# Kernel tuning notes

Hardware: AMD Instinct MI355X
Metric: run time of the kernel (lower is better)

## Reference

```python
import jax, jax.numpy as jnp
import numpy as np

N = 50000       # nodes
E = 800000      # edges (before self-loops)
IN_DIM = 8
H = 4           # heads (layers 1-2)
D = 32          # per-head hidden dim
HD = H * D      # 128
BN_EPS = 1e-5
NEG_SLOPE = 0.2


def _gat_conv(x, src, dst, W, a_src, a_dst, b, heads, concat):
    """PyG-style GATConv (eval mode, self-loops already in src/dst)."""
    n = x.shape[0]
    h = (x @ W).reshape(n, heads, -1)                      # [N, H, D]
    al_s = jnp.einsum('nhd,hd->nh', h, a_src)              # [N, H]
    al_d = jnp.einsum('nhd,hd->nh', h, a_dst)              # [N, H]
    e = jax.nn.leaky_relu(al_s[src] + al_d[dst], NEG_SLOPE)  # [E', H]
    m = jax.ops.segment_max(e, dst, num_segments=n)
    m = jnp.where(jnp.isfinite(m), m, 0.0)
    ex = jnp.exp(e - m[dst])
    den = jax.ops.segment_sum(ex, dst, num_segments=n)
    alpha = ex / (den[dst] + 1e-16)                        # [E', H] neighborhood softmax
    out = jax.ops.segment_sum(alpha[:, :, None] * h[src], dst, num_segments=n)  # [N, H, D]
    out = out.reshape(n, -1) if concat else out.mean(axis=1)
    return out + b


def _bn(x, g, b, m, v):
    return (x - m) * jax.lax.rsqrt(v + BN_EPS) * g + b


def setup_inputs() -> dict:
    key = jax.random.key(0)
    ks = jax.random.split(key, 32)
    f32 = jnp.float32
    d = {}
    d['x'] = jax.random.normal(ks[0], (N, IN_DIM), dtype=f32)
    d['edge_index'] = jax.random.randint(ks[1], (2, E), 0, N, dtype=jnp.int64)
    # layer 1: GAT(8 -> 32, 4 heads, concat)
    d['W1'] = jax.random.normal(ks[2], (IN_DIM, HD), dtype=f32) * 0.3
    d['as1'] = jax.random.normal(ks[3], (H, D), dtype=f32) * 0.3
    d['ad1'] = jax.random.normal(ks[4], (H, D), dtype=f32) * 0.3
    d['b1'] = jax.random.normal(ks[5], (HD,), dtype=f32) * 0.1
    d['g1'] = 1.0 + 0.1 * jax.random.normal(ks[6], (HD,), dtype=f32)
    d['be1'] = 0.1 * jax.random.normal(ks[7], (HD,), dtype=f32)
    d['m1'] = 0.1 * jax.random.normal(ks[8], (HD,), dtype=f32)
    d['v1'] = jax.random.uniform(ks[9], (HD,), dtype=f32, minval=0.5, maxval=1.5)
    # layer 2: GAT(128 -> 32, 4 heads, concat)
    d['W2'] = jax.random.normal(ks[10], (HD, HD), dtype=f32) * 0.1
    d['as2'] = jax.random.normal(ks[11], (H, D), dtype=f32) * 0.3
    d['ad2'] = jax.random.normal(ks[12], (H, D), dtype=f32) * 0.3
    d['b2'] = jax.random.normal(ks[13], (HD,), dtype=f32) * 0.1
    d['g2'] = 1.0 + 0.1 * jax.random.normal(ks[14], (HD,), dtype=f32)
    d['be2'] = 0.1 * jax.random.normal(ks[15], (HD,), dtype=f32)
    d['m2'] = 0.1 * jax.random.normal(ks[16], (HD,), dtype=f32)
    d['v2'] = jax.random.uniform(ks[17], (HD,), dtype=f32, minval=0.5, maxval=1.5)
    # layer 3: GAT(128 -> 32, 1 head, no concat)
    d['W3'] = jax.random.normal(ks[18], (HD, D), dtype=f32) * 0.1
    d['as3'] = jax.random.normal(ks[19], (1, D), dtype=f32) * 0.3
    d['ad3'] = jax.random.normal(ks[20], (1, D), dtype=f32) * 0.3
    d['b3'] = jax.random.normal(ks[21], (D,), dtype=f32) * 0.1
    d['g3'] = 1.0 + 0.1 * jax.random.normal(ks[22], (D,), dtype=f32)
    d['be3'] = 0.1 * jax.random.normal(ks[23], (D,), dtype=f32)
    d['m3'] = 0.1 * jax.random.normal(ks[24], (D,), dtype=f32)
    d['v3'] = jax.random.uniform(ks[25], (D,), dtype=f32, minval=0.5, maxval=1.5)
    # classifier: Linear(32->16) -> ReLU -> Linear(16->1)
    d['cW1'] = jax.random.normal(ks[26], (D, 16), dtype=f32) * 0.2
    d['cb1'] = 0.1 * jax.random.normal(ks[27], (16,), dtype=f32)
    d['cW2'] = jax.random.normal(ks[28], (16, 1), dtype=f32) * 0.2
    d['cb2'] = 0.1 * jax.random.normal(ks[29], (1,), dtype=f32)
    return d


def reference(x, edge_index, W1, as1, ad1, b1, g1, be1, m1, v1,
              W2, as2, ad2, b2, g2, be2, m2, v2,
              W3, as3, ad3, b3, g3, be3, m3, v3,
              cW1, cb1, cW2, cb2):
    n = x.shape[0]
    loop = jnp.arange(n, dtype=edge_index.dtype)
    src = jnp.concatenate([edge_index[0], loop])   # PyG adds self-loops
    dst = jnp.concatenate([edge_index[1], loop])
    x1 = jax.nn.elu(_bn(_gat_conv(x, src, dst, W1, as1, ad1, b1, H, True), g1, be1, m1, v1))
    x2 = jax.nn.elu(_bn(_gat_conv(x1, src, dst, W2, as2, ad2, b2, H, True), g2, be2, m2, v2))
    x3 = jax.nn.elu(_bn(_gat_conv(x2, src, dst, W3, as3, ad3, b3, 1, False), g3, be3, m3, v3))
    hidden = jax.nn.relu(x3 @ cW1 + cb1)
    return jax.nn.sigmoid(hidden @ cW2 + cb2)      # [N, 1]
```

## Files before the change

kernel.cpp:

```cpp
#include <hip/hip_runtime.h>
#include <hip/hip_bf16.h>

#define BN_EPS 1e-5f
#define CAPB 6144
#define LOG2E 1.4426950408889634f

typedef unsigned short ushort_t;
typedef __attribute__((ext_vector_type(2))) float f32x2;

__device__ __forceinline__ float blo(unsigned w) { unsigned t = w << 16; return __builtin_bit_cast(float, t); }
__device__ __forceinline__ float bhi(unsigned w) { unsigned t = w & 0xffff0000u; return __builtin_bit_cast(float, t); }
__device__ __forceinline__ unsigned packbf2(float a, float b) {
  unsigned lo = (unsigned)__builtin_bit_cast(unsigned short, __float2bfloat16(a));
  unsigned hi = (unsigned)__builtin_bit_cast(unsigned short, __float2bfloat16(b));
  return lo | (hi << 16);
}
__device__ __forceinline__ float fexp2(float x) {
#if __has_builtin(__builtin_amdgcn_exp2f)
  return __builtin_amdgcn_exp2f(x);
#else
  return exp2f(x);
#endif
}
__device__ __forceinline__ void pkfma(f32x2& d, f32x2 a, f32x2 b) {
  asm("v_pk_fma_f32 %0, %1, %2, %0" : "+v"(d) : "v"(a), "v"(b));
}


__global__ __launch_bounds__(256) void k_binit(int* __restrict__ gCur, int nb) {
  int i = blockIdx.x * 256 + threadIdx.x;
  if (i < nb) gCur[i] = i * CAPB;
}

__global__ __launch_bounds__(256) void k_bucket(const int* __restrict__ ei, int E, int etot,
                                                unsigned* __restrict__ bkt, int* __restrict__ gCur,
                                                int nb) {
  __shared__ int sm[256];
  __shared__ int lstart[256];
  __shared__ int lcur[256];
  __shared__ int gbase[256];
  __shared__ unsigned stage[1024];
  int tid = threadIdx.x;
  int base = blockIdx.x * 1024;
  int cnt = etot - base; if (cnt > 1024) cnt = 1024;

  sm[tid] = 0;
  __syncthreads();
  unsigned key[4]; int have[4];
  #pragma unroll
  for (int u = 0; u < 4; ++u) {
    int idx = tid + u * 256;
    have[u] = (idx < cnt);
    if (have[u]) {
      int i = base + idx;
      int s, d;
      if (i < E) { s = ei[i]; d = ei[E + i]; }
      else       { s = i - E; d = s; }
      unsigned k = ((unsigned)d << 16) | (unsigned)s;
      key[u] = k;
      atomicAdd(&sm[k >> 24], 1);
    }
  }
  __syncthreads();
  int myc = sm[tid];
  #pragma unroll
  for (int off = 1; off < 256; off <<= 1) {
    int t = sm[tid];
    int u = (tid >= off) ? sm[tid - off] : 0;
    __syncthreads();
    sm[tid] = t + u;
    __syncthreads();
  }
  int excl = sm[tid] - myc;
  lstart[tid] = excl;
  lcur[tid] = excl;
  if (tid < nb) gbase[tid] = atomicAdd(&gCur[tid], myc);
  __syncthreads();
  #pragma unroll
  for (int u = 0; u < 4; ++u) {
    if (have[u]) {
      int bin = key[u] >> 24;
      int pos = atomicAdd(&lcur[bin], 1);
      stage[pos] = key[u];
    }
  }
  __syncthreads();
  for (int j = tid; j < cnt; j += 256) {
    unsigned k = stage[j];
    int bin = k >> 24;
    bkt[(size_t)gbase[bin] + (j - lstart[bin])] = k;
  }
}

__global__ __launch_bounds__(256) void k_csr(const unsigned* __restrict__ bkt,
                                             const int* __restrict__ gCur,
                                             int* __restrict__ csr, int* __restrict__ offs,
                                             int n, int nb, int etot) {
  __shared__ int sm[256];
  __shared__ int lstart[256];
  __shared__ int lcur[256];
  __shared__ unsigned itm[CAPB];
  __shared__ ushort_t limg[CAPB];
  int tid = threadIdx.x, b = blockIdx.x;
  int cnt = gCur[b] - b * CAPB;

  int c = 0;
  if (tid < nb) c = gCur[tid] - tid * CAPB;
  sm[tid] = c;
  __syncthreads();
  #pragma unroll
  for (int off = 1; off < 256; off <<= 1) {
    int t = sm[tid];
    int u = (tid >= off) ? sm[tid - off] : 0;
    __syncthreads();
    sm[tid] = t + u;
    __syncthreads();
  }
  int gbase = sm[b] - cnt;
  __syncthreads();

  sm[tid] = 0;
  __syncthreads();
  for (int j = tid; j < cnt; j += 256) {
    unsigned k = bkt[(size_t)b * CAPB + j];
    itm[j] = k;
    atomicAdd(&sm[(k >> 16) & 255], 1);
  }
  __syncthreads();
  int myc = sm[tid];
  #pragma unroll
  for (int off = 1; off < 256; off <<= 1) {
    int t = sm[tid];
    int u = (tid >= off) ? sm[tid - off] : 0;
    __syncthreads();
    sm[tid] = t + u;
    __syncthreads();
  }
  int excl = sm[tid] - myc;
  lstart[tid] = excl;
  lcur[tid] = excl;
  __syncthreads();
  for (int j = tid; j < cnt; j += 256) {
    unsigned k = itm[j];
    int d = (k >> 16) & 255;
    int pos = atomicAdd(&lcur[d], 1);
    limg[pos] = (ushort_t)(k & 0xffffu);
  }
  __syncthreads();
  for (int j = tid; j < cnt; j += 256) csr[gbase + j] = (int)limg[j];
  int gd = b * 256 + tid;
  if (gd < n) offs[gd] = gbase + lstart[tid];
  if (b == nb - 1 && tid == 0) offs[n] = etot;
}


template<int K, int FOUT, int HEADS, int BK>
__global__ __launch_bounds__(256) void k_gemm_t(const float* __restrict__ X,
    const float* __restrict__ W, const float* __restrict__ a_s, const float* __restrict__ a_d,
    ushort_t* __restrict__ Hout, float* __restrict__ als, float* __restrict__ ald, int n) {
  constexpr int BM = 128;
  constexpr int CT = FOUT / 8;
  constexpr int RT = 256 / CT;
  constexpr int TM = BM / RT;
  __shared__ float Xl[BK][BM];
  __shared__ float Wl[BK][FOUT];

  int tid = threadIdx.x;
  int ct = tid % CT, rt = tid / CT;
  int row0 = blockIdx.x * BM;

  float acc[TM][8];
  #pragma unroll
  for (int i = 0; i < TM; ++i)
    #pragma unroll
    for (int j = 0; j < 8; ++j) acc[i][j] = 0.f;

  for (int k0 = 0; k0 < K; k0 += BK) {
    constexpr int TPR = BK / 4;
    for (int s = tid; s < BM * TPR; s += 256) {
      int r = s / TPR, c4 = (s % TPR) * 4;
      float4 v = make_float4(0.f, 0.f, 0.f, 0.f);
      int grow = row0 + r;
      if (grow < n) v = *(const float4*)&X[(size_t)grow * K + k0 + c4];
      Xl[c4 + 0][r] = v.x; Xl[c4 + 1][r] = v.y; Xl[c4 + 2][r] = v.z; Xl[c4 + 3][r] = v.w;
    }
    for (int s = tid; s < BK * (FOUT / 4); s += 256) {
      int kk = s / (FOUT / 4), c4 = (s % (FOUT / 4)) * 4;
      *(float4*)&Wl[kk][c4] = *(const float4*)&W[(size_t)(k0 + kk) * FOUT + c4];
    }
    __syncthreads();
    #pragma unroll
    for (int kk = 0; kk < BK; ++kk) {
      float b[8], a[TM];
      *(float4*)&b[0] = *(const float4*)&Wl[kk][ct * 8];
      *(float4*)&b[4] = *(const float4*)&Wl[kk][ct * 8 + 4];
      #pragma unroll
      for (int i4 = 0; i4 < TM; i4 += 4)
        *(float4*)&a[i4] = *(const float4*)&Xl[kk][rt * TM + i4];
      #pragma unroll
      for (int i = 0; i < TM; ++i)
        #pragma unroll
        for (int j = 0; j < 8; ++j) acc[i][j] += a[i] * b[j];
    }
    __syncthreads();
  }

  int col0 = ct * 8;
  int head = (HEADS == 4) ? (col0 >> 5) : 0;
  float asv[8], adv[8];
  #pragma unroll
  for (int j = 0; j < 8; ++j) {
    asv[j] = a_s[head * 32 + ((col0 + j) & 31)] * LOG2E;
    adv[j] = a_d[head * 32 + ((col0 + j) & 31)] * LOG2E;
  }
  #pragma unroll
  for (int i = 0; i < TM; ++i) {
    int row = row0 + rt * TM + i;
    if (row >= n) break;
    uint4 pk;
    pk.x = packbf2(acc[i][0], acc[i][1]);
    pk.y = packbf2(acc[i][2], acc[i][3]);
    pk.z = packbf2(acc[i][4], acc[i][5]);
    pk.w = packbf2(acc[i][6], acc[i][7]);
    *(uint4*)&Hout[(size_t)row * FOUT + col0] = pk;
    float ps = 0.f, pd = 0.f;
    #pragma unroll
    for (int j = 0; j < 8; ++j) { ps += acc[i][j] * asv[j]; pd += acc[i][j] * adv[j]; }
    ps += __shfl_xor(ps, 1, 64); ps += __shfl_xor(ps, 2, 64);
    pd += __shfl_xor(pd, 1, 64); pd += __shfl_xor(pd, 2, 64);
    if ((ct & 3) == 0) {
      als[row * HEADS + head] = ps;
      ald[row * HEADS + head] = pd;
    }
  }
}


__device__ __forceinline__ int sel4(int eg, int a, int b, int c, int d) {
  int r = (eg & 1) ? b : a;
  int r2 = (eg & 1) ? d : c;
  return (eg & 2) ? r2 : r;
}

__global__ __launch_bounds__(256) void k_agg4(const int* __restrict__ offs, const int* __restrict__ csr,
    const ushort_t* __restrict__ Hb, const float* __restrict__ als, const float* __restrict__ ald,
    const float* __restrict__ bias, const float* __restrict__ gam, const float* __restrict__ bet,
    const float* __restrict__ mu, const float* __restrict__ var,
    float* __restrict__ Xo, int n) {
  constexpr int UB = 6;
  constexpr int CAPW = 252;
  __shared__ int   s_idx[4][CAPW];
  __shared__ float s_exp[4][CAPW * 4];
  int wslot = threadIdx.x >> 6;
  int wid = (blockIdx.x * 256 + threadIdx.x) >> 6;
  int v0 = wid * 4;
  if (v0 >= n) return;
  int lane = threadIdx.x & 63;

  int va = v0, vb = min(v0 + 1, n), vc = min(v0 + 2, n), vd = min(v0 + 3, n);
  int o0 = offs[va], o1 = offs[vb], o2 = offs[vc], o3 = offs[vd], o4 = offs[min(v0 + 4, n)];
  int d0 = o1 - o0, d1 = o2 - o1, d2 = o3 - o2, d3 = o4 - o3;

  int room = CAPW;
  int ms0 = min(d0, room); int mp0 = min((ms0 + UB - 1) / UB * UB, room); ms0 = min(ms0, mp0); room -= mp0;
  int ms1 = min(d1, room); int mp1 = min((ms1 + UB - 1) / UB * UB, room); ms1 = min(ms1, mp1); room -= mp1;
  int ms2 = min(d2, room); int mp2 = min((ms2 + UB - 1) / UB * UB, room); ms2 = min(ms2, mp2); room -= mp2;
  int ms3 = min(d3, room); int mp3 = min((ms3 + UB - 1) / UB * UB, room); ms3 = min(ms3, mp3);
  int p0 = 0, p1 = mp0, p2 = mp0 + mp1, p3 = mp0 + mp1 + mp2;

  int total = o4 - o0;
  for (int l = lane; l < total; l += 64) {
    int j = o0 + l;
    int nd = (j >= o1) + (j >= o2) + (j >= o3);
    int cbase = sel4(nd, o0 - p0, o1 - p1, o2 - p2, o3 - p3);
    int lim   = sel4(nd, p0 + ms0, p1 + ms1, p2 + ms2, p3 + ms3);
    int pos = j - cbase;
    if (pos < lim) {
      int s = csr[j];
      s_idx[wslot][pos] = s << 8;
      const float4 av = *(const float4*)&als[(size_t)s * 4];
      const float4 dv = *(const float4*)&ald[(size_t)(v0 + nd) * 4];
      float e0 = av.x + dv.x, e1 = av.y + dv.y, e2 = av.z + dv.z, e3 = av.w + dv.w;
      e0 = fmaxf(e0, 0.2f * e0); e1 = fmaxf(e1, 0.2f * e1);
      e2 = fmaxf(e2, 0.2f * e2); e3 = fmaxf(e3, 0.2f * e3);
      *(float4*)&s_exp[wslot][pos * 4] = make_float4(fexp2(e0), fexp2(e1), fexp2(e2), fexp2(e3));
    }
  }
  if (lane < 4 * UB) {
    int v = lane / UB, q = lane % UB;
    int msv = sel4(v, ms0, ms1, ms2, ms3);
    int mpv = sel4(v, mp0, mp1, mp2, mp3);
    int pv  = sel4(v, p0, p1, p2, p3);
    if (q < mpv - msv) {
      int pos = pv + msv + q;
      s_idx[wslot][pos] = 0;
      *(float4*)&s_exp[wslot][pos * 4] = make_float4(0.f, 0.f, 0.f, 0.f);
    }
  }

  int eg = lane >> 4;
  int fl = lane & 15;
  int f0 = fl * 8;
  int myh = f0 >> 5;
  int st  = sel4(eg, p0, p1, p2, p3);
  int mpv = sel4(eg, mp0, mp1, mp2, mp3);
  int msv = sel4(eg, ms0, ms1, ms2, ms3);
  int dgv = sel4(eg, d0, d1, d2, d3);
  int obv = sel4(eg, o0, o1, o2, o3);
  const char* hb = (const char*)Hb + f0 * 2;

  f32x2 acc2[4];
  #pragma unroll
  for (int q = 0; q < 4; ++q) acc2[q] = (f32x2){0.f, 0.f};
  float den = 0.f;

  for (int j0 = 0; j0 < mpv; j0 += UB) {
    int ss[UB]; float ex[UB];
    #pragma unroll
    for (int u = 0; u < UB; ++u) {
      int pidx = st + j0 + u;
      ss[u] = s_idx[wslot][pidx];
      ex[u] = s_exp[wslot][pidx * 4 + myh];
    }
    uint4 pv[UB];
    #pragma unroll
    for (int u = 0; u < UB; ++u)
      pv[u] = *(const uint4*)(hb + (size_t)(unsigned)ss[u]);
    #pragma unroll
    for (int u = 0; u < UB; ++u) {
      f32x2 e2v = (f32x2){ex[u], ex[u]};
      f32x2 h0 = (f32x2){blo(pv[u].x), bhi(pv[u].x)};
      f32x2 h1 = (f32x2){blo(pv[u].y), bhi(pv[u].y)};
      f32x2 h2 = (f32x2){blo(pv[u].z), bhi(pv[u].z)};
      f32x2 h3 = (f32x2){blo(pv[u].w), bhi(pv[u].w)};
      pkfma(acc2[0], e2v, h0);
      pkfma(acc2[1], e2v, h1);
      pkfma(acc2[2], e2v, h2);
      pkfma(acc2[3], e2v, h3);
    }
    den += ((ex[0] + ex[1]) + (ex[2] + ex[3])) + (ex[4] + ex[5]);
  }
  if (dgv > msv) {
    float myald = ald[(size_t)(v0 + eg) * 4 + myh];
    for (int j = msv; j < dgv; ++j) {
      int s = csr[obv + j];
      float e = als[(size_t)s * 4 + myh] + myald;
      e = fmaxf(e, 0.2f * e);
      float exv = fexp2(e);
      den += exv;
      uint4 pv = *(const uint4*)(Hb + (size_t)s * 128 + f0);
      f32x2 e2v = (f32x2){exv, exv};
      pkfma(acc2[0], e2v, (f32x2){blo(pv.x), bhi(pv.x)});
      pkfma(acc2[1], e2v, (f32x2){blo(pv.y), bhi(pv.y)});
      pkfma(acc2[2], e2v, (f32x2){blo(pv.z), bhi(pv.z)});
      pkfma(acc2[3], e2v, (f32x2){blo(pv.w), bhi(pv.w)});
    }
  }

  int node = v0 + eg;
  if (node >= n) return;
  float acc[8] = {acc2[0].x, acc2[0].y, acc2[1].x, acc2[1].y,
                  acc2[2].x, acc2[2].y, acc2[3].x, acc2[3].y};
  float inv = 1.f / (den + 1e-16f);
  float4 bi0 = *(const float4*)&bias[f0], bi1 = *(const float4*)&bias[f0 + 4];
  float4 mu0 = *(const float4*)&mu[f0],   mu1 = *(const float4*)&mu[f0 + 4];
  float4 va0 = *(const float4*)&var[f0],  va1 = *(const float4*)&var[f0 + 4];
  float4 ga0 = *(const float4*)&gam[f0],  ga1 = *(const float4*)&gam[f0 + 4];
  float4 be0 = *(const float4*)&bet[f0],  be1 = *(const float4*)&bet[f0 + 4];
  float bb[8] = {bi0.x, bi0.y, bi0.z, bi0.w, bi1.x, bi1.y, bi1.z, bi1.w};
  float mm[8] = {mu0.x, mu0.y, mu0.z, mu0.w, mu1.x, mu1.y, mu1.z, mu1.w};
  float vv[8] = {va0.x, va0.y, va0.z, va0.w, va1.x, va1.y, va1.z, va1.w};
  float gg[8] = {ga0.x, ga0.y, ga0.z, ga0.w, ga1.x, ga1.y, ga1.z, ga1.w};
  float ee[8] = {be0.x, be0.y, be0.z, be0.w, be1.x, be1.y, be1.z, be1.w};
  float ov[8];
  #pragma unroll
  for (int q = 0; q < 8; ++q) {
    float xo = acc[q] * inv + bb[q];
    xo = (xo - mm[q]) * rsqrtf(vv[q] + BN_EPS) * gg[q] + ee[q];
    ov[q] = (xo > 0.f) ? xo : (__expf(xo) - 1.f);
  }
  *(float4*)(Xo + (size_t)node * 128 + f0)     = make_float4(ov[0], ov[1], ov[2], ov[3]);
  *(float4*)(Xo + (size_t)node * 128 + f0 + 4) = make_float4(ov[4], ov[5], ov[6], ov[7]);
}


__global__ __launch_bounds__(256) void k_agg1(const int* __restrict__ offs, const int* __restrict__ csr,
    const ushort_t* __restrict__ Hb, const float* __restrict__ als, const float* __restrict__ ald,
    const float* __restrict__ bias, const float* __restrict__ gam, const float* __restrict__ bet,
    const float* __restrict__ mu, const float* __restrict__ var,
    float* __restrict__ Xo, int n) {
  constexpr int LPF = 4;
  constexpr int EPW = 16;
  constexpr int UB = 2;
  constexpr int STEP = 32;
  constexpr int CAP = 128;
  __shared__ int   s_idx[4][CAP];
  __shared__ float s_exp[4][CAP];
  int wslot = threadIdx.x >> 6;
  int wv = (blockIdx.x * 256 + threadIdx.x) >> 6;
  if (wv >= n) return;
  int lane = threadIdx.x & 63;
  int rs = offs[wv];
  int deg = offs[wv + 1] - rs;
  int dstage = deg < CAP ? deg : CAP;
  int dpad = ((dstage + STEP - 1) / STEP) * STEP;
  float ald0 = ald[wv];

  for (int j = lane; j < dpad; j += 64) {
    if (j < dstage) {
      int s = csr[rs + j];
      s_idx[wslot][j] = s << 6;
      float e = als[s] + ald0;
      e = fmaxf(e, 0.2f * e);
      s_exp[wslot][j] = fexp2(e);
    } else {
      s_idx[wslot][j] = 0;
      s_exp[wslot][j] = 0.f;
    }
  }

  int fl = lane % LPF;
  int eg = lane / LPF;
  int f0 = fl * 8;
  const char* hb = (const char*)Hb + f0 * 2;

  f32x2 acc2[4];
  #pragma unroll
  for (int q = 0; q < 4; ++q) acc2[q] = (f32x2){0.f, 0.f};
  float den = 0.f;

  for (int j0 = eg; j0 < dpad; j0 += STEP) {
    int ss[UB]; float ex[UB];
    #pragma unroll
    for (int u = 0; u < UB; ++u) {
      int j = j0 + u * EPW;
      ss[u] = s_idx[wslot][j];
      ex[u] = s_exp[wslot][j];
    }
    uint4 pv[UB];
    #pragma unroll
    for (int u = 0; u < UB; ++u)
      pv[u] = *(const uint4*)(hb + (size_t)(unsigned)ss[u]);
    #pragma unroll
    for (int u = 0; u < UB; ++u) {
      f32x2 e2v = (f32x2){ex[u], ex[u]};
      pkfma(acc2[0], e2v, (f32x2){blo(pv[u].x), bhi(pv[u].x)});
      pkfma(acc2[1], e2v, (f32x2){blo(pv[u].y), bhi(pv[u].y)});
      pkfma(acc2[2], e2v, (f32x2){blo(pv[u].z), bhi(pv[u].z)});
      pkfma(acc2[3], e2v, (f32x2){blo(pv[u].w), bhi(pv[u].w)});
      den += ex[u];
    }
  }
  if (deg > CAP) {
    for (int j = CAP + eg; j < deg; j += EPW) {
      int s = csr[rs + j];
      float e = als[s] + ald0;
      e = fmaxf(e, 0.2f * e);
      float exv = fexp2(e);
      den += exv;
      uint4 pv = *(const uint4*)(Hb + (size_t)s * 32 + f0);
      f32x2 e2v = (f32x2){exv, exv};
      pkfma(acc2[0], e2v, (f32x2){blo(pv.x), bhi(pv.x)});
      pkfma(acc2[1], e2v, (f32x2){blo(pv.y), bhi(pv.y)});
      pkfma(acc2[2], e2v, (f32x2){blo(pv.z), bhi(pv.z)});
      pkfma(acc2[3], e2v, (f32x2){blo(pv.w), bhi(pv.w)});
    }
  }

  float acc[8] = {acc2[0].x, acc2[0].y, acc2[1].x, acc2[1].y,
                  acc2[2].x, acc2[2].y, acc2[3].x, acc2[3].y};
  #pragma unroll
  for (int off = 32; off >= LPF; off >>= 1) {
    den += __shfl_xor(den, off, 64);
    #pragma unroll
    for (int q = 0; q < 8; ++q) acc[q] += __shfl_xor(acc[q], off, 64);
  }
  float inv = 1.f / (den + 1e-16f);

  if (lane < LPF) {
    float ov[8];
    #pragma unroll
    for (int q = 0; q < 8; ++q) {
      int f = f0 + q;
      float xo = acc[q] * inv + bias[f];
      xo = (xo - mu[f]) * rsqrtf(var[f] + BN_EPS) * gam[f] + bet[f];
      ov[q] = (xo > 0.f) ? xo : (__expf(xo) - 1.f);
    }
    *(float4*)(Xo + (size_t)wv * 32 + f0)     = make_float4(ov[0], ov[1], ov[2], ov[3]);
    *(float4*)(Xo + (size_t)wv * 32 + f0 + 4) = make_float4(ov[4], ov[5], ov[6], ov[7]);
  }
}


__global__ __launch_bounds__(256) void k_cls(const float* __restrict__ X3,
    const float* __restrict__ cW1, const float* __restrict__ cb1,
    const float* __restrict__ cW2, const float* __restrict__ cb2,
    float* __restrict__ out, int n) {
  int i = blockIdx.x * 256 + threadIdx.x;
  if (i >= n) return;
  float x[32];
  #pragma unroll
  for (int k = 0; k < 32; k += 4) {
    float4 v = *(const float4*)&X3[(size_t)i * 32 + k];
    x[k] = v.x; x[k + 1] = v.y; x[k + 2] = v.z; x[k + 3] = v.w;
  }
  float o = cb2[0];
  #pragma unroll
  for (int j = 0; j < 16; ++j) {
    float hs = cb1[j];
    #pragma unroll
    for (int k = 0; k < 32; ++k) hs += x[k] * cW1[k * 16 + j];
    hs = fmaxf(hs, 0.f);
    o += hs * cW2[j];
  }
  out[i] = 1.f / (1.f + __expf(-o));
}


static inline size_t align256(size_t x) { return (x + 255) & ~(size_t)255; }

extern "C" void kernel_launch(void* const* d_in, const int* in_sizes, int n_in,
                              void* d_out, int out_size, void* d_ws, size_t ws_size,
                              hipStream_t stream) {
  const float* x   = (const float*)d_in[0];
  const int*   ei  = (const int*)d_in[1];
  const float* W1  = (const float*)d_in[2];
  const float* as1 = (const float*)d_in[3];
  const float* ad1 = (const float*)d_in[4];
  const float* b1  = (const float*)d_in[5];
  const float* g1  = (const float*)d_in[6];
  const float* be1 = (const float*)d_in[7];
  const float* m1  = (const float*)d_in[8];
  const float* v1  = (const float*)d_in[9];
  const float* W2  = (const float*)d_in[10];
  const float* as2 = (const float*)d_in[11];
  const float* ad2 = (const float*)d_in[12];
  const float* b2  = (const float*)d_in[13];
  const float* g2  = (const float*)d_in[14];
  const float* be2 = (const float*)d_in[15];
  const float* m2  = (const float*)d_in[16];
  const float* v2  = (const float*)d_in[17];
  const float* W3  = (const float*)d_in[18];
  const float* as3 = (const float*)d_in[19];
  const float* ad3 = (const float*)d_in[20];
  const float* b3  = (const float*)d_in[21];
  const float* g3  = (const float*)d_in[22];
  const float* be3 = (const float*)d_in[23];
  const float* m3  = (const float*)d_in[24];
  const float* v3  = (const float*)d_in[25];
  const float* cW1 = (const float*)d_in[26];
  const float* cb1 = (const float*)d_in[27];
  const float* cW2 = (const float*)d_in[28];
  const float* cb2 = (const float*)d_in[29];

  const int n = in_sizes[0] / 8;
  const int E = in_sizes[1] / 2;
  const int etot = E + n;
  const int nb = (n + 255) / 256;

  char* p = (char*)d_ws;
  int* offs   = (int*)p;  p += align256((size_t)(n + 1) * 4);
  int* csr    = (int*)p;  p += align256((size_t)etot * 4);
  int* gCur   = (int*)p;  p += align256(1024);
  unsigned* bkt = (unsigned*)p; p += align256((size_t)nb * CAPB * 4);
  float* als  = (float*)p; p += align256((size_t)n * 4 * 4);
  float* ald  = (float*)p; p += align256((size_t)n * 4 * 4);
  ushort_t* bufH = (ushort_t*)p; p += align256((size_t)n * 128 * 2);
  float* bufX = (float*)p; p += align256((size_t)n * 128 * 4);

  k_binit<<<(nb + 255) / 256, 256, 0, stream>>>(gCur, nb);
  k_bucket<<<(etot + 1023) / 1024, 256, 0, stream>>>(ei, E, etot, bkt, gCur, nb);
  k_csr<<<nb, 256, 0, stream>>>(bkt, gCur, csr, offs, n, nb, etot);

  const int gt = (n + 127) / 128;
  const int ga4 = (n + 15) / 16;
  const int ga1 = (n + 3) / 4;

  k_gemm_t<8, 128, 4, 8><<<gt, 256, 0, stream>>>(x, W1, as1, ad1, bufH, als, ald, n);
  k_agg4<<<ga4, 256, 0, stream>>>(offs, csr, bufH, als, ald, b1, g1, be1, m1, v1, bufX, n);

  k_gemm_t<128, 128, 4, 16><<<gt, 256, 0, stream>>>(bufX, W2, as2, ad2, bufH, als, ald, n);
  k_agg4<<<ga4, 256, 0, stream>>>(offs, csr, bufH, als, ald, b2, g2, be2, m2, v2, bufX, n);

  k_gemm_t<128, 32, 1, 16><<<gt, 256, 0, stream>>>(bufX, W3, as3, ad3, bufH, als, ald, n);
  k_agg1<<<ga1, 256, 0, stream>>>(offs, csr, bufH, als, ald, b3, g3, be3, m3, v3, bufX, n);

  k_cls<<<(n + 255) / 256, 256, 0, stream>>>(bufX, cW1, cb1, cW2, cb2, (float*)d_out, n);
}
```

Baseline: 206.0 us.

## Use bf16 MFMA GEMMs for layers 2-3 with bf16 intermediate activations

Layers 2 and 3 now use a new MFMA-based GEMM (16x16x32 bf16) that reads bf16 activations and pre-transposed bf16 weights. A small kernel converts W2 and W3 to transposed bf16 on every call. The layer 1 and layer 2 aggregation outputs are stored as bf16 instead of fp32, which halves activation traffic, and layer 3 writes to a separate fp32 buffer for the classifier. This replaces scalar FP32 FMA work with matrix-core work, at the cost of lower activation and weight precision and one extra small launch.

```diff
diff --git a/kernel.cpp b/kernel.cpp
--- a/kernel.cpp
+++ b/kernel.cpp
@@ -7,12 +7,17 @@
 
 typedef unsigned short ushort_t;
 typedef __attribute__((ext_vector_type(2))) float f32x2;
+typedef __attribute__((ext_vector_type(4))) float f32x4v;
+typedef __attribute__((ext_vector_type(8))) short short8;
 
 __device__ __forceinline__ float blo(unsigned w) { unsigned t = w << 16; return __builtin_bit_cast(float, t); }
 __device__ __forceinline__ float bhi(unsigned w) { unsigned t = w & 0xffff0000u; return __builtin_bit_cast(float, t); }
+__device__ __forceinline__ ushort_t bfbits(float a) {
+  return (ushort_t)__builtin_bit_cast(unsigned short, __float2bfloat16(a));
+}
 __device__ __forceinline__ unsigned packbf2(float a, float b) {
-  unsigned lo = (unsigned)__builtin_bit_cast(unsigned short, __float2bfloat16(a));
-  unsigned hi = (unsigned)__builtin_bit_cast(unsigned short, __float2bfloat16(b));
+  unsigned lo = (unsigned)bfbits(a);
+  unsigned hi = (unsigned)bfbits(b);
   return lo | (hi << 16);
 }
 __device__ __forceinline__ float fexp2(float x) {
@@ -154,6 +159,21 @@
 }
 
 
+__global__ __launch_bounds__(256) void k_wconv(const float* __restrict__ W2, const float* __restrict__ W3,
+                                               ushort_t* __restrict__ Wt2, ushort_t* __restrict__ Wt3) {
+  int t = blockIdx.x * 256 + threadIdx.x;
+  const int np = 128 * 128;
+  if (t < np) {
+    int c = t / 128, k = t % 128;
+    Wt2[t] = bfbits(W2[k * 128 + c]);
+  } else if (t < np + 32 * 128) {
+    int i = t - np;
+    int c = i / 128, k = i % 128;
+    Wt3[i] = bfbits(W3[k * 32 + c]);
+  }
+}
+
+
 template<int K, int FOUT, int HEADS, int BK>
 __global__ __launch_bounds__(256) void k_gemm_t(const float* __restrict__ X,
     const float* __restrict__ W, const float* __restrict__ a_s, const float* __restrict__ a_d,
@@ -236,6 +256,99 @@
 }
 
 
+template<int FOUT>
+__global__ __launch_bounds__(256) void k_gemm_mfma(
+    const ushort_t* __restrict__ X, const ushort_t* __restrict__ Wt,
+    const float* __restrict__ a_s, const float* __restrict__ a_d,
+    ushort_t* __restrict__ Hout, float* __restrict__ als, float* __restrict__ ald, int n) {
+  constexpr int HEADS = FOUT / 32;
+  constexpr int BM = (FOUT == 128) ? 64 : 256;
+  constexpr int LDC = FOUT + 8;
+  __shared__ ushort_t Ct[BM * LDC];
+  int tid = threadIdx.x;
+  int w = tid >> 6, lane = tid & 63;
+  int lo = lane & 15, hi = lane >> 4;
+  int rowB = blockIdx.x * BM;
+  int row0 = (FOUT == 128) ? rowB : rowB + w * 64;
+  int nbase = (FOUT == 128) ? w * 32 : 0;
+  int h = (FOUT == 128) ? w : 0;
+
+  f32x4v acc[4][2];
+  #pragma unroll
+  for (int mf = 0; mf < 4; ++mf)
+    #pragma unroll
+    for (int nf = 0; nf < 2; ++nf) acc[mf][nf] = (f32x4v){0.f, 0.f, 0.f, 0.f};
+
+  #pragma unroll
+  for (int k0 = 0; k0 < 4; ++k0) {
+    int kof = k0 * 32 + hi * 8;
+    short8 b[2];
+    #pragma unroll
+    for (int nf = 0; nf < 2; ++nf) {
+      int col = nbase + nf * 16 + lo;
+      b[nf] = *(const short8*)&Wt[(size_t)col * 128 + kof];
+    }
+    short8 a[4];
+    #pragma unroll
+    for (int mf = 0; mf < 4; ++mf) {
+      int row = row0 + mf * 16 + lo;
+      row = min(row, n - 1);
+      a[mf] = *(const short8*)&X[(size_t)row * 128 + kof];
+    }
+    #pragma unroll
+    for (int mf = 0; mf < 4; ++mf)
+      #pragma unroll
+      for (int nf = 0; nf < 2; ++nf)
+        acc[mf][nf] = __builtin_amdgcn_mfma_f32_16x16x32_bf16(a[mf], b[nf], acc[mf][nf], 0, 0, 0);
+  }
+
+  float as0 = a_s[h * 32 + lo] * LOG2E, as1 = a_s[h * 32 + 16 + lo] * LOG2E;
+  float ad0 = a_d[h * 32 + lo] * LOG2E, ad1 = a_d[h * 32 + 16 + lo] * LOG2E;
+  #pragma unroll
+  for (int mf = 0; mf < 4; ++mf) {
+    #pragma unroll
+    for (int j = 0; j < 4; ++j) {
+      float ps = acc[mf][0][j] * as0 + acc[mf][1][j] * as1;
+      float pd = acc[mf][0][j] * ad0 + acc[mf][1][j] * ad1;
+      #pragma unroll
+      for (int m = 1; m < 16; m <<= 1) {
+        ps += __shfl_xor(ps, m, 64);
+        pd += __shfl_xor(pd, m, 64);
+      }
+      if (lo == 0) {
+        int row = row0 + mf * 16 + hi * 4 + j;
+        if (row < n) {
+          als[(size_t)row * HEADS + h] = ps;
+          ald[(size_t)row * HEADS + h] = pd;
+        }
+      }
+    }
+  }
+
+  #pragma unroll
+  for (int mf = 0; mf < 4; ++mf) {
+    int rL = ((FOUT == 128) ? 0 : w * 64) + mf * 16 + hi * 4;
+    #pragma unroll
+    for (int nf = 0; nf < 2; ++nf) {
+      int cL = nbase + nf * 16 + lo;
+      #pragma unroll
+      for (int j = 0; j < 4; ++j)
+        Ct[(rL + j) * LDC + cL] = bfbits(acc[mf][nf][j]);
+    }
+  }
+  __syncthreads();
+  constexpr int CPR = FOUT / 8;
+  #pragma unroll
+  for (int i = 0; i < (BM * CPR) / 256; ++i) {
+    int idx = tid + i * 256;
+    int r = idx / CPR, c = idx % CPR;
+    int grow = rowB + r;
+    if (grow < n)
+      *(uint4*)&Hout[(size_t)grow * FOUT + c * 8] = *(const uint4*)&Ct[r * LDC + c * 8];
+  }
+}
+
+
 __device__ __forceinline__ int sel4(int eg, int a, int b, int c, int d) {
   int r = (eg & 1) ? b : a;
   int r2 = (eg & 1) ? d : c;
@@ -246,7 +359,7 @@
     const ushort_t* __restrict__ Hb, const float* __restrict__ als, const float* __restrict__ ald,
     const float* __restrict__ bias, const float* __restrict__ gam, const float* __restrict__ bet,
     const float* __restrict__ mu, const float* __restrict__ var,
-    float* __restrict__ Xo, int n) {
+    ushort_t* __restrict__ Xo, int n) {
   constexpr int UB = 6;
   constexpr int CAPW = 252;
   __shared__ int   s_idx[4][CAPW];
@@ -329,14 +442,10 @@
     #pragma unroll
     for (int u = 0; u < UB; ++u) {
       f32x2 e2v = (f32x2){ex[u], ex[u]};
-      f32x2 h0 = (f32x2){blo(pv[u].x), bhi(pv[u].x)};
-      f32x2 h1 = (f32x2){blo(pv[u].y), bhi(pv[u].y)};
-      f32x2 h2 = (f32x2){blo(pv[u].z), bhi(pv[u].z)};
-      f32x2 h3 = (f32x2){blo(pv[u].w), bhi(pv[u].w)};
-      pkfma(acc2[0], e2v, h0);
-      pkfma(acc2[1], e2v, h1);
-      pkfma(acc2[2], e2v, h2);
-      pkfma(acc2[3], e2v, h3);
+      pkfma(acc2[0], e2v, (f32x2){blo(pv[u].x), bhi(pv[u].x)});
+      pkfma(acc2[1], e2v, (f32x2){blo(pv[u].y), bhi(pv[u].y)});
+      pkfma(acc2[2], e2v, (f32x2){blo(pv[u].z), bhi(pv[u].z)});
+      pkfma(acc2[3], e2v, (f32x2){blo(pv[u].w), bhi(pv[u].w)});
     }
     den += ((ex[0] + ex[1]) + (ex[2] + ex[3])) + (ex[4] + ex[5]);
   }
@@ -379,8 +488,10 @@
     xo = (xo - mm[q]) * rsqrtf(vv[q] + BN_EPS) * gg[q] + ee[q];
     ov[q] = (xo > 0.f) ? xo : (__expf(xo) - 1.f);
   }
-  *(float4*)(Xo + (size_t)node * 128 + f0)     = make_float4(ov[0], ov[1], ov[2], ov[3]);
-  *(float4*)(Xo + (size_t)node * 128 + f0 + 4) = make_float4(ov[4], ov[5], ov[6], ov[7]);
+  uint4 pk;
+  pk.x = packbf2(ov[0], ov[1]); pk.y = packbf2(ov[2], ov[3]);
+  pk.z = packbf2(ov[4], ov[5]); pk.w = packbf2(ov[6], ov[7]);
+  *(uint4*)&Xo[(size_t)node * 128 + f0] = pk;
 }
 
 
@@ -566,11 +677,15 @@
   float* als  = (float*)p; p += align256((size_t)n * 4 * 4);
   float* ald  = (float*)p; p += align256((size_t)n * 4 * 4);
   ushort_t* bufH = (ushort_t*)p; p += align256((size_t)n * 128 * 2);
-  float* bufX = (float*)p; p += align256((size_t)n * 128 * 4);
+  ushort_t* bufX = (ushort_t*)p; p += align256((size_t)n * 128 * 2);
+  float* x3f  = (float*)p; p += align256((size_t)n * 32 * 4);
+  ushort_t* wt2 = (ushort_t*)p; p += align256(128 * 128 * 2);
+  ushort_t* wt3 = (ushort_t*)p; p += align256(32 * 128 * 2);
 
   k_binit<<<(nb + 255) / 256, 256, 0, stream>>>(gCur, nb);
   k_bucket<<<(etot + 1023) / 1024, 256, 0, stream>>>(ei, E, etot, bkt, gCur, nb);
   k_csr<<<nb, 256, 0, stream>>>(bkt, gCur, csr, offs, n, nb, etot);
+  k_wconv<<<80, 256, 0, stream>>>(W2, W3, wt2, wt3);
 
   const int gt = (n + 127) / 128;
   const int ga4 = (n + 15) / 16;
@@ -579,11 +694,11 @@
   k_gemm_t<8, 128, 4, 8><<<gt, 256, 0, stream>>>(x, W1, as1, ad1, bufH, als, ald, n);
   k_agg4<<<ga4, 256, 0, stream>>>(offs, csr, bufH, als, ald, b1, g1, be1, m1, v1, bufX, n);
 
-  k_gemm_t<128, 128, 4, 16><<<gt, 256, 0, stream>>>(bufX, W2, as2, ad2, bufH, als, ald, n);
+  k_gemm_mfma<128><<<(n + 63) / 64, 256, 0, stream>>>(bufX, wt2, as2, ad2, bufH, als, ald, n);
   k_agg4<<<ga4, 256, 0, stream>>>(offs, csr, bufH, als, ald, b2, g2, be2, m2, v2, bufX, n);
 
-  k_gemm_t<128, 32, 1, 16><<<gt, 256, 0, stream>>>(bufX, W3, as3, ad3, bufH, als, ald, n);
-  k_agg1<<<ga1, 256, 0, stream>>>(offs, csr, bufH, als, ald, b3, g3, be3, m3, v3, bufX, n);
-
-  k_cls<<<(n + 255) / 256, 256, 0, stream>>>(bufX, cW1, cb1, cW2, cb2, (float*)d_out, n);
-}
+  k_gemm_mfma<32><<<(n + 255) / 256, 256, 0, stream>>>(bufX, wt3, as3, ad3, bufH, als, ald, n);
+  k_agg1<<<ga1, 256, 0, stream>>>(offs, csr, bufH, als, ald, b3, g3, be3, m3, v3, x3f, n);
+
+  k_cls<<<(n + 255) / 256, 256, 0, stream>>>(x3f, cW1, cb1, cW2, cb2, (float*)d_out, n);
+}
```

Result: faster. 185.2 us (-10.1%).
